# Kernel optimization log

Measured on AMD Instinct MI355X. Metric: run time of the kernel, lower is better.

Reference implementation:

```python
import jax, jax.numpy as jnp
import numpy as np

_SQRT1_2 = 0.7071067811865476

B, S, D, N, NCH = 4, 2048, 1024, 32768, 8


def setup_inputs() -> dict:
    key = jax.random.key(0)
    ks = jax.random.split(key, 6)
    return {
        "x": jax.random.normal(ks[0], (B, S, D), jnp.float32),
        "h": jax.random.normal(ks[1], (B, S, D), jnp.float32),
        "emb": jax.random.normal(ks[2], (N, D), jnp.float32),
        "tau_offset": jax.random.normal(ks[3], (B, S, 1), jnp.float32),
        "w_read": jax.random.normal(ks[4], (N, D), jnp.float32),
        "w_write": jax.random.normal(ks[5], (N, D), jnp.float32),
        "n_chunks": NCH,
    }


def _srw_chunked(x, h, emb_unit, tau_offset, w_read, w_write, n_chunks):
    b, s, d = x.shape
    n = emb_unit.shape[0]
    cs = n // n_chunks
    h_bf = h.astype(jnp.bfloat16)
    x_bf = x.astype(jnp.bfloat16)
    emb_bf = emb_unit.astype(jnp.bfloat16)
    read_bf = w_read.astype(jnp.bfloat16)
    write_bf = w_write.astype(jnp.bfloat16)
    z1 = jnp.zeros((b, s, 1), jnp.float32)

    # ---- pass 1: online score statistics over chunks of N ----
    @jax.checkpoint
    def stats_step(carry, i):
        s_sum, sq_sum, cube_sum, ns_sum, ns_sq = carry
        ec = jax.lax.dynamic_slice_in_dim(emb_bf, i * cs, cs, axis=0)
        sc = (h_bf @ ec.T).astype(jnp.float32)  # [B,S,cs]
        s_sum = s_sum + sc.sum(-1, keepdims=True)
        sq_sum = sq_sum + (sc ** 2).sum(-1, keepdims=True)
        cube_sum = cube_sum + (sc ** 3).sum(-1, keepdims=True)
        pns = sc.mean(axis=(0, 1))  # per-neuron mean score [cs]
        return ((s_sum, sq_sum, cube_sum, ns_sum + pns.sum(), ns_sq + (pns ** 2).sum()), None)

    (s_sum, sq_sum, cube_sum, ns_sum, ns_sq), _ = jax.lax.scan(
        stats_step, (z1, z1, z1, jnp.float32(0.0), jnp.float32(0.0)), jnp.arange(n_chunks))

    s_mean = s_sum / n
    s_std = jnp.sqrt(sq_sum / n - s_mean ** 2) + 1e-08
    tau = s_mean + tau_offset * s_std
    cube_mean = cube_sum / n
    central_third = cube_mean - 3.0 * s_mean * s_std ** 2 - s_mean ** 3
    score_skew = jax.lax.stop_gradient((central_third / (s_std ** 3 + 1e-08)).mean())
    mean_score = ns_sum / n
    var_score = ns_sq / n - mean_score ** 2
    score_lb = var_score / (mean_score ** 2 + var_score + 0.01)

    # ---- pass 2: erf-threshold gate + read/write GEMM accumulate ----
    @jax.checkpoint
    def gate_step(carry, i):
        out, wcost, gmax, act, strong, phib, zsum, z075c, z030c, glg = carry
        s0 = i * cs
        ec = jax.lax.dynamic_slice_in_dim(emb_bf, s0, cs, axis=0)
        rc = jax.lax.dynamic_slice_in_dim(read_bf, s0, cs, axis=0)
        wc = jax.lax.dynamic_slice_in_dim(write_bf, s0, cs, axis=0)
        rc = rc / (jnp.linalg.norm(rc, axis=-1, keepdims=True) + 1e-08)
        wc = wc / (jnp.linalg.norm(wc, axis=-1, keepdims=True) + 1e-08)
        z = ((h_bf @ ec.T).astype(jnp.float32) - tau) / s_std  # [B,S,cs]
        phi = 0.5 * (1.0 + jax.lax.erf(z * _SQRT1_2))
        gate = jnp.where(z > 0, z * phi, 0.0)
        xr = x_bf @ rc.T  # [B,S,cs]
        c_out = ((gate.astype(jnp.bfloat16) * xr) @ wc).astype(jnp.float32)  # [B,S,D]
        g_safe = gate + 1e-08
        new = (
            out + c_out,
            wcost + gate.sum(-1, keepdims=True),
            jnp.maximum(gmax, gate.max(-1, keepdims=True)),
            act + (gate > 0.0).astype(jnp.float32).sum(-1, keepdims=True),
            strong + (gate > 0.5).astype(jnp.float32).sum(-1, keepdims=True),
            phib + ((phi > 0.95) | (phi < 0.05)).astype(jnp.float32).sum(-1, keepdims=True),
            zsum + jnp.where(z > 0, z, 0.0).sum(-1, keepdims=True),
            z075c + ((z > 0) & (z < 0.75)).astype(jnp.float32).sum(-1, keepdims=True),
            z030c + ((z > 0) & (z < 0.3)).astype(jnp.float32).sum(-1, keepdims=True),
            glg + (gate * jnp.log(g_safe)).sum(-1, keepdims=True),
        )
        return (new, None)

    init = (jnp.zeros((b, s, d), jnp.float32), z1, jnp.full((b, s, 1), -1e9, jnp.float32),
            z1, z1, z1, z1, z1, z1, z1)
    (raw_out, wcost, gmax, act, strong, phib, zsum, z075c, z030c, glg), _ = jax.lax.scan(
        gate_step, init, jnp.arange(n_chunks))

    den = jnp.maximum(wcost, 1.0)
    out = (raw_out / den).astype(jnp.bfloat16)
    score_std_out = s_std.mean()
    es_out = wcost.mean()
    active_n_mean = act.mean()
    z_mean_active = zsum / (act + 1e-08)
    active_eps = act + 1e-08
    z_lt_075_frac = jax.lax.stop_gradient((z075c / active_eps).mean())
    z_lt_030_frac = jax.lax.stop_gradient((z030c / active_eps).mean())
    tau_abs_mean = jax.lax.stop_gradient(tau).mean()
    active_per_token_std = jax.lax.stop_gradient(act).std()
    gate_sum_eps = wcost + 1e-08
    entropy_per_token = -glg / gate_sum_eps + jnp.log(gate_sum_eps)
    gate_entropy = jax.lax.stop_gradient(entropy_per_token).mean()
    return (out.astype(jnp.float32), act / n, gmax, score_lb, score_std_out, es_out,
            active_n_mean, strong / n, phib / n, z_mean_active, tau_abs_mean,
            z_lt_075_frac, z_lt_030_frac, score_skew, active_per_token_std, gate_entropy)


def reference(x, h, emb, tau_offset, w_read, w_write, n_chunks):
    emb_unit = emb / (jnp.linalg.norm(emb, axis=-1, keepdims=True) + 1e-08)
    return _srw_chunked(x, h, emb_unit, tau_offset, w_read, w_write, n_chunks)
```

## Files before the change

kernel.cpp:

```cpp
#include <hip/hip_runtime.h>

#define DEV __device__ __forceinline__

typedef __attribute__((ext_vector_type(4))) float f32x4;
typedef __attribute__((ext_vector_type(8))) short s16x8;
typedef __attribute__((ext_vector_type(8))) unsigned short u16x8;

static const int NTOK = 8192;
static const int DD   = 1024;
static const int NNEU = 32768;
static const int NC   = 8192;

static const int OUT_ACT    = 8388608;
static const int OUT_GMAX   = 8396800;
static const int OUT_SLB    = 8404992;
static const int OUT_SSTD   = 8404993;
static const int OUT_ES     = 8404994;
static const int OUT_ANM    = 8404995;
static const int OUT_STRONG = 8404996;
static const int OUT_PHIB   = 8413188;
static const int OUT_ZMEAN  = 8421380;
static const int OUT_TAUM   = 8429572;
static const int OUT_Z75    = 8429573;
static const int OUT_Z30    = 8429574;
static const int OUT_SKEW   = 8429575;
static const int OUT_ASTD   = 8429576;
static const int OUT_ENT    = 8429577;

DEV unsigned short f2bf(float f){
  unsigned u = __float_as_uint(f);
  u += 0x7fffu + ((u >> 16) & 1u);
  return (unsigned short)(u >> 16);
}
DEV float bf2f(unsigned short h){ return __uint_as_float(((unsigned)h) << 16); }
DEV float rnd_bf(float f){ return bf2f(f2bf(f)); }

template<int AUX>
DEV void gl_lds16(const void* g, void* l){
  __builtin_amdgcn_global_load_lds(
      (const __attribute__((address_space(1))) unsigned int*)g,
      (__attribute__((address_space(3))) unsigned int*)l, 16, 0, AUX);
}

DEV f32x4 mfma16(s16x8 a, s16x8 b, f32x4 c){
  return __builtin_amdgcn_mfma_f32_16x16x32_bf16(a, b, c, 0, 0, 0);
}

template<int AUX>
DEV void stage4(const unsigned short* __restrict__ G, size_t ld, int k0,
                unsigned short* L, int t){
  #pragma unroll
  for (int i = 0; i < 4; i++){
    int ch = i*256 + t;
    int row = ch >> 3, c = ch & 7;
    int cs = c ^ (row & 7);
    int wb = (i*256 + (t & 192)) * 16;
    gl_lds16<AUX>(G + (size_t)row * ld + k0 + cs*8, (char*)L + wb);
  }
}

DEV s16x8 frg(const unsigned short* L, int R, int kk, int lq){
  int cc = ((kk >> 3) + lq) ^ (R & 7);
  return *(const s16x8*)((const char*)L + R*128 + cc*16);
}

DEV void waitv_bar(){
  asm volatile("s_waitcnt vmcnt(0)" ::: "memory");
  __builtin_amdgcn_s_barrier();
  __builtin_amdgcn_sched_barrier(0);
}

DEV int2 xcd_remap(){
  int orig = blockIdx.y * gridDim.x + blockIdx.x;
  int nwg  = gridDim.x * gridDim.y;
  int q = nwg >> 3;
  int xcd = orig & 7, idx = orig >> 3;
  int pos = xcd * q + idx;
  int2 r; r.x = pos >> 6; r.y = pos & 63;
  return r;
}


__global__ __launch_bounds__(256) void k_norms(const float* __restrict__ e,
    const float* __restrict__ r_, const float* __restrict__ w_,
    float* __restrict__ inv_e, float* __restrict__ inv_r, float* __restrict__ inv_w){
  int t = threadIdx.x, l = t & 63, wv = t >> 6;
  int row = blockIdx.x * 4 + wv;
  const float4* ep = (const float4*)(e  + (size_t)row * DD);
  const float4* rp = (const float4*)(r_ + (size_t)row * DD);
  const float4* wp = (const float4*)(w_ + (size_t)row * DD);
  float se = 0.f, sr = 0.f, sw = 0.f;
  #pragma unroll
  for (int j = 0; j < 4; j++){
    float4 v = ep[j*64 + l];
    se += v.x*v.x + v.y*v.y + v.z*v.z + v.w*v.w;
    float4 a = rp[j*64 + l];
    float a0 = rnd_bf(a.x), a1 = rnd_bf(a.y), a2 = rnd_bf(a.z), a3 = rnd_bf(a.w);
    sr += a0*a0 + a1*a1 + a2*a2 + a3*a3;
    float4 c = wp[j*64 + l];
    float c0 = rnd_bf(c.x), c1 = rnd_bf(c.y), c2 = rnd_bf(c.z), c3 = rnd_bf(c.w);
    sw += c0*c0 + c1*c1 + c2*c2 + c3*c3;
  }
  #pragma unroll
  for (int d = 1; d < 64; d <<= 1){
    se += __shfl_xor(se, d); sr += __shfl_xor(sr, d); sw += __shfl_xor(sw, d);
  }
  if (l == 0){
    inv_e[row] = 1.f / (sqrtf(se) + 1e-8f);
    inv_r[row] = 1.f / (sqrtf(sr) + 1e-8f);
    inv_w[row] = 1.f / (sqrtf(sw) + 1e-8f);
  }
}

__global__ __launch_bounds__(256) void k_cast_scale(const float* __restrict__ in,
    const float* __restrict__ inv, unsigned short* __restrict__ o, int round_first){
  size_t i = (size_t)blockIdx.x * 256 + threadIdx.x;
  int row = (int)(i >> 8);
  float s = inv[row];
  float4 v = ((const float4*)in)[i];
  ushort4 r;
  if (round_first){
    r.x = f2bf(rnd_bf(v.x) * s); r.y = f2bf(rnd_bf(v.y) * s);
    r.z = f2bf(rnd_bf(v.z) * s); r.w = f2bf(rnd_bf(v.w) * s);
  } else {
    r.x = f2bf(v.x * s); r.y = f2bf(v.y * s);
    r.z = f2bf(v.z * s); r.w = f2bf(v.w * s);
  }
  ((ushort4*)o)[i] = r;
}

__global__ __launch_bounds__(256) void k_cast(const float* __restrict__ in,
                                              unsigned short* __restrict__ o){
  size_t i = (size_t)blockIdx.x * 256 + threadIdx.x;
  float4 v = ((const float4*)in)[i];
  ushort4 r;
  r.x = f2bf(v.x); r.y = f2bf(v.y); r.z = f2bf(v.z); r.w = f2bf(v.w);
  ((ushort4*)o)[i] = r;
}

__global__ __launch_bounds__(256) void k_wcnT(const float* __restrict__ w_,
    const float* __restrict__ invw, unsigned short* __restrict__ o){
  __shared__ unsigned short tile[64][65];
  int t = threadIdx.x;
  int n0b = blockIdx.x * 64, d0 = blockIdx.y * 64;
  #pragma unroll
  for (int i = 0; i < 16; i++){
    int idx = t + i*256;
    int r = idx >> 6, c = idx & 63;
    float v = w_[(size_t)(n0b + r) * DD + d0 + c];
    tile[c][r] = f2bf(rnd_bf(v) * invw[n0b + r]);
  }
  __syncthreads();
  #pragma unroll
  for (int i = 0; i < 16; i++){
    int idx = t + i*256;
    int rd = idx >> 6, cn = idx & 63;
    o[(size_t)(d0 + rd) * NNEU + n0b + cn] = tile[rd][cn];
  }
}

__global__ __launch_bounds__(256) void k_hsum(const unsigned short* __restrict__ hb,
                                              float* __restrict__ hs){
  int t = threadIdx.x; int r0 = blockIdx.x * 128;
  float s[4] = {0.f, 0.f, 0.f, 0.f};
  for (int r = 0; r < 128; r++){
    const unsigned short* row = hb + (size_t)(r0 + r) * DD;
    #pragma unroll
    for (int j = 0; j < 4; j++) s[j] += bf2f(row[j*256 + t]);
  }
  #pragma unroll
  for (int j = 0; j < 4; j++) atomicAdd(hs + j*256 + t, s[j]);
}

__global__ __launch_bounds__(256) void k_pns(const unsigned short* __restrict__ eb,
    const float* __restrict__ hs, float* __restrict__ ns){
  __shared__ float hsh[1024];
  __shared__ float pr[8];
  int t = threadIdx.x, l = t & 63, wv = t >> 6;
  for (int i = t; i < 1024; i += 256) hsh[i] = hs[i];
  __syncthreads();
  float bs = 0.f, bq = 0.f;
  for (int it = 0; it < 32; it++){
    int row = blockIdx.x * 128 + it*4 + wv;
    const unsigned short* er = eb + (size_t)row * DD + l*16;
    float s = 0.f;
    #pragma unroll
    for (int j = 0; j < 16; j++) s += hsh[l*16 + j] * bf2f(er[j]);
    #pragma unroll
    for (int d = 1; d < 64; d <<= 1) s += __shfl_xor(s, d);
    float pns = s * (1.f / 8192.f);
    bs += pns; bq += pns * pns;
  }
  if (l == 0){ pr[wv*2] = bs; pr[wv*2 + 1] = bq; }
  __syncthreads();
  if (t == 0){
    atomicAdd(ns + 0, pr[0] + pr[2] + pr[4] + pr[6]);
    atomicAdd(ns + 1, pr[1] + pr[3] + pr[5] + pr[7]);
  }
}


__global__ __launch_bounds__(256, 2) void k_stats_gemm(
    const unsigned short* __restrict__ A, const unsigned short* __restrict__ Bm,
    float* __restrict__ s_sum, float* __restrict__ sq_sum, float* __restrict__ cu_sum,
    unsigned short* __restrict__ Sb, int kst)
{
  __shared__ unsigned short lds[32768];
  const int t = threadIdx.x, l = t & 63, wv = t >> 6;
  const int wm = wv >> 1, wn = wv & 1;
  const int lq = l >> 4, lr = l & 15;
  int2 rm = xcd_remap();
  const int bx = rm.x, by = rm.y;
  const unsigned short* Ab = A  + (size_t)by * 128 * DD;
  const unsigned short* Bb = Bm + (size_t)bx * 128 * DD;
  f32x4 acc[4][4];
  #pragma unroll
  for (int m = 0; m < 4; m++)
    #pragma unroll
    for (int n = 0; n < 4; n++) acc[m][n] = (f32x4){0.f, 0.f, 0.f, 0.f};

  stage4<0>(Ab, DD, 0, lds, t);
  stage4<0>(Bb, DD, 0, lds + 8192, t);
  waitv_bar();
  int cur = 0;
  for (int ks = 0; ks < 16; ++ks){
    unsigned short* Lc = lds + cur*16384;
    if (ks + 1 < 16){
      unsigned short* Ln = lds + (cur^1)*16384;
      int k0 = (ks+1)*64;
      stage4<0>(Ab, DD, k0, Ln, t);
      stage4<0>(Bb, DD, k0, Ln + 8192, t);
    }
    #pragma unroll
    for (int kk = 0; kk < 64; kk += 32){
      s16x8 af[4], bf4[4];
      #pragma unroll
      for (int m = 0; m < 4; m++) af[m]  = frg(Lc, wm*64 + m*16 + lr, kk, lq);
      #pragma unroll
      for (int n = 0; n < 4; n++) bf4[n] = frg(Lc + 8192, wn*64 + n*16 + lr, kk, lq);
      #pragma unroll
      for (int m = 0; m < 4; m++)
        #pragma unroll
        for (int n = 0; n < 4; n++)
          acc[m][n] = mfma16(af[m], bf4[n], acc[m][n]);
    }
    waitv_bar();
    cur ^= 1;
  }

  int ci = bx >> 6;
  if (ci < kst){
    unsigned short* sl = lds;
    #pragma unroll
    for (int m = 0; m < 4; m++)
    #pragma unroll
    for (int n = 0; n < 4; n++)
    #pragma unroll
    for (int r = 0; r < 4; r++){
      int rl = wm*64 + m*16 + lq*4 + r;
      int cl = wn*64 + n*16 + lr;
      sl[rl*136 + cl] = f2bf(acc[m][n][r]);
    }
    __syncthreads();
    unsigned short* Sp = Sb + (size_t)ci * NTOK * NC;
    int bxc = bx & 63;
    #pragma unroll
    for (int i = 0; i < 8; i++){
      int idx = i*2048 + t*8;
      int row = idx >> 7, col = idx & 127;
      u16x8 v = *(const u16x8*)&sl[row*136 + col];
      __builtin_nontemporal_store(v,
        (u16x8*)(Sp + (size_t)(by*128 + row) * NC + bxc*128 + col));
    }
  }
  __syncthreads();

  float* red = (float*)lds;
  #pragma unroll
  for (int m = 0; m < 4; m++)
  #pragma unroll
  for (int r = 0; r < 4; r++){
    float s1 = 0.f, s2 = 0.f, s3 = 0.f;
    #pragma unroll
    for (int n = 0; n < 4; n++){
      float v = rnd_bf(acc[m][n][r]);
      s1 += v; float v2 = v*v; s2 += v2; s3 += v2*v;
    }
    #pragma unroll
    for (int d = 1; d < 16; d <<= 1){
      s1 += __shfl_xor(s1, d); s2 += __shfl_xor(s2, d); s3 += __shfl_xor(s3, d);
    }
    if (lr == 0){
      int rl = wm*64 + m*16 + lq*4 + r;
      float* p = red + (wn*128 + rl)*4;
      p[0] = s1; p[1] = s2; p[2] = s3;
    }
  }
  __syncthreads();
  const int row0 = by * 128;
  for (int idx = t; idx < 384; idx += 256){
    int rl = idx / 3, st = idx - rl*3;
    float v = red[rl*4 + st] + red[(128 + rl)*4 + st];
    float* dst = (st == 0) ? s_sum : (st == 1) ? sq_sum : cu_sum;
    atomicAdd(dst + row0 + rl, v);
  }
}

__global__ __launch_bounds__(256) void k_tau(const float* __restrict__ s_sum,
    const float* __restrict__ sq_sum, const float* __restrict__ tof,
    float* __restrict__ tau, float* __restrict__ rstd){
  int i = blockIdx.x * 256 + threadIdx.x;
  float mean = s_sum[i] * (1.f / 32768.f);
  float var  = sq_sum[i] * (1.f / 32768.f) - mean*mean;
  float sstd = sqrtf(fmaxf(var, 0.f)) + 1e-8f;
  tau[i]  = mean + tof[i] * sstd;
  rstd[i] = 1.f / sstd;
}


__global__ __launch_bounds__(256, 2) void k_gateS(
    const unsigned short* __restrict__ Xb, const unsigned short* __restrict__ Rb,
    const float* __restrict__ tau, const float* __restrict__ rstd,
    unsigned short* __restrict__ SP, int n0,
    float* __restrict__ wcostp, float* __restrict__ gmaxp, float* __restrict__ actp,
    float* __restrict__ strongp, float* __restrict__ phibp, float* __restrict__ zsump,
    float* __restrict__ z075p, float* __restrict__ z030p, float* __restrict__ glgp)
{
  __shared__ unsigned short lds[32768];
  const int t = threadIdx.x, l = t & 63, wv = t >> 6;
  const int wm = wv >> 1, wn = wv & 1;
  const int lq = l >> 4, lr = l & 15;
  int2 rm = xcd_remap();
  const int bx = rm.x, by = rm.y;
  const unsigned short* Xp = Xb + (size_t)by * 128 * DD;
  const unsigned short* Rp = Rb + (size_t)(n0 + bx*128) * DD;
  f32x4 accX[4][4];
  #pragma unroll
  for (int m = 0; m < 4; m++)
    #pragma unroll
    for (int n = 0; n < 4; n++) accX[m][n] = (f32x4){0.f,0.f,0.f,0.f};

  stage4<0>(Xp, DD, 0, lds, t);
  stage4<0>(Rp, DD, 0, lds + 8192, t);
  waitv_bar();
  int cur = 0;
  for (int ks = 0; ks < 16; ++ks){
    unsigned short* Lc = lds + cur*16384;
    if (ks + 1 < 16){
      unsigned short* Ln = lds + (cur^1)*16384;
      int k0 = (ks+1)*64;
      stage4<0>(Xp, DD, k0, Ln, t);
      stage4<0>(Rp, DD, k0, Ln + 8192, t);
    }
    #pragma unroll
    for (int kk = 0; kk < 64; kk += 32){
      s16x8 af[4], bf4[4];
      #pragma unroll
      for (int m = 0; m < 4; m++) af[m]  = frg(Lc, wm*64 + m*16 + lr, kk, lq);
      #pragma unroll
      for (int n = 0; n < 4; n++) bf4[n] = frg(Lc + 8192, wn*64 + n*16 + lr, kk, lq);
      #pragma unroll
      for (int m = 0; m < 4; m++)
        #pragma unroll
        for (int n = 0; n < 4; n++)
          accX[m][n] = mfma16(af[m], bf4[n], accX[m][n]);
    }
    waitv_bar();
    cur ^= 1;
  }

  unsigned short sv[4][4][4];
  #pragma unroll
  for (int m = 0; m < 4; m++)
  #pragma unroll
  for (int r = 0; r < 4; r++)
  #pragma unroll
  for (int n = 0; n < 4; n++){
    int gr = by*128 + wm*64 + m*16 + lq*4 + r;
    int gc = bx*128 + wn*64 + n*16 + lr;
    sv[m][r][n] = SP[(size_t)gr * NC + gc];
  }

  __syncthreads();
  float* red = (float*)lds;
  #pragma unroll
  for (int m = 0; m < 4; m++)
  #pragma unroll
  for (int r = 0; r < 4; r++){
    int rl = wm*64 + m*16 + lq*4 + r;
    int gr = by*128 + rl;
    float tauv = tau[gr], rs = rstd[gr];
    float wsum = 0.f, gmx = 0.f, ac = 0.f, stc = 0.f, pb = 0.f;
    float zs = 0.f, z7 = 0.f, z3 = 0.f, gl = 0.f;
    #pragma unroll
    for (int n = 0; n < 4; n++){
      float sc = bf2f(sv[m][r][n]);
      float xr = rnd_bf(accX[m][n][r]);
      float z = (sc - tauv) * rs;
      float phi = 0.5f * (1.0f + erff(z * 0.70710678118654752440f));
      float gate = (z > 0.f) ? z * phi : 0.f;
      wsum += gate; gmx = fmaxf(gmx, gate);
      if (gate > 0.f)  ac  += 1.f;
      if (gate > 0.5f) stc += 1.f;
      if (phi > 0.95f || phi < 0.05f) pb += 1.f;
      if (z > 0.f){ zs += z; if (z < 0.75f) z7 += 1.f; if (z < 0.3f) z3 += 1.f; }
      gl += gate * __logf(gate + 1e-8f);
      float p = rnd_bf(gate) * xr;
      SP[(size_t)gr * NC + bx*128 + wn*64 + n*16 + lr] = f2bf(p);
    }
    #pragma unroll
    for (int d = 1; d < 16; d <<= 1){
      wsum += __shfl_xor(wsum, d); gmx = fmaxf(gmx, __shfl_xor(gmx, d));
      ac += __shfl_xor(ac, d);  stc += __shfl_xor(stc, d); pb += __shfl_xor(pb, d);
      zs += __shfl_xor(zs, d);  z7  += __shfl_xor(z7, d);  z3 += __shfl_xor(z3, d);
      gl += __shfl_xor(gl, d);
    }
    if (lr == 0){
      float* p = red + (wn*128 + rl)*10;
      p[0]=wsum; p[1]=gmx; p[2]=ac; p[3]=stc; p[4]=pb; p[5]=zs; p[6]=z7; p[7]=z3; p[8]=gl;
    }
  }
  __syncthreads();
  for (int idx = t; idx < 1152; idx += 256){
    int rl = idx / 9, st = idx - rl*9;
    float a = red[rl*10 + st], b = red[(128 + rl)*10 + st];
    int gr = by*128 + rl;
    if (st == 1){
      atomicMax((int*)(gmaxp + gr), __float_as_int(fmaxf(a, b)));
    } else {
      float v = a + b;
      float* dst = (st==0)?wcostp:(st==2)?actp:(st==3)?strongp:(st==4)?phibp:
                   (st==5)?zsump:(st==6)?z075p:(st==7)?z030p:glgp;
      atomicAdd(dst + gr, v);
    }
  }
}


__global__ __launch_bounds__(256, 2) void k_gate_gemm(
    const unsigned short* __restrict__ Hb, const unsigned short* __restrict__ Eb,
    const unsigned short* __restrict__ Xb, const unsigned short* __restrict__ Rb,
    const float* __restrict__ tau, const float* __restrict__ rstd,
    unsigned short* __restrict__ P, int n0,
    float* __restrict__ wcostp, float* __restrict__ gmaxp, float* __restrict__ actp,
    float* __restrict__ strongp, float* __restrict__ phibp, float* __restrict__ zsump,
    float* __restrict__ z075p, float* __restrict__ z030p, float* __restrict__ glgp)
{
  __shared__ unsigned short lds[32768];
  unsigned short* lH = lds;
  unsigned short* lE = lds + 8192;
  unsigned short* lX = lds + 16384;
  unsigned short* lR = lds + 24576;
  const int t = threadIdx.x, l = t & 63, wv = t >> 6;
  const int wm = wv >> 1, wn = wv & 1;
  const int lq = l >> 4, lr = l & 15;
  int2 rm = xcd_remap();
  const int bx = rm.x, by = rm.y;
  const unsigned short* Hp = Hb + (size_t)by * 128 * DD;
  const unsigned short* Xp = Xb + (size_t)by * 128 * DD;
  const unsigned short* Ep = Eb + (size_t)(n0 + bx*128) * DD;
  const unsigned short* Rp = Rb + (size_t)(n0 + bx*128) * DD;
  f32x4 accS[4][4], accX[4][4];
  #pragma unroll
  for (int m = 0; m < 4; m++)
    #pragma unroll
    for (int n = 0; n < 4; n++){
      accS[m][n] = (f32x4){0.f,0.f,0.f,0.f};
      accX[m][n] = (f32x4){0.f,0.f,0.f,0.f};
    }

  for (int k0 = 0; k0 < DD; k0 += 64){
    __syncthreads();
    stage4<0>(Hp, DD, k0, lH, t);
    stage4<0>(Ep, DD, k0, lE, t);
    stage4<0>(Xp, DD, k0, lX, t);
    stage4<0>(Rp, DD, k0, lR, t);
    asm volatile("s_waitcnt vmcnt(0)" ::: "memory");
    __syncthreads();
    #pragma unroll
    for (int kk = 0; kk < 64; kk += 32){
      s16x8 af[4], bf4[4];
      #pragma unroll
      for (int m = 0; m < 4; m++) af[m]  = frg(lH, wm*64 + m*16 + lr, kk, lq);
      #pragma unroll
      for (int n = 0; n < 4; n++) bf4[n] = frg(lE, wn*64 + n*16 + lr, kk, lq);
      #pragma unroll
      for (int m = 0; m < 4; m++)
        #pragma unroll
        for (int n = 0; n < 4; n++)
          accS[m][n] = mfma16(af[m], bf4[n], accS[m][n]);
      #pragma unroll
      for (int m = 0; m < 4; m++) af[m]  = frg(lX, wm*64 + m*16 + lr, kk, lq);
      #pragma unroll
      for (int n = 0; n < 4; n++) bf4[n] = frg(lR, wn*64 + n*16 + lr, kk, lq);
      #pragma unroll
      for (int m = 0; m < 4; m++)
        #pragma unroll
        for (int n = 0; n < 4; n++)
          accX[m][n] = mfma16(af[m], bf4[n], accX[m][n]);
    }
  }
  __syncthreads();
  float* red = (float*)lds;
  #pragma unroll
  for (int m = 0; m < 4; m++)
  #pragma unroll
  for (int r = 0; r < 4; r++){
    int rl = wm*64 + m*16 + lq*4 + r;
    int gr = by*128 + rl;
    float tauv = tau[gr], rs = rstd[gr];
    float wsum = 0.f, gmx = 0.f, ac = 0.f, stc = 0.f, pb = 0.f;
    float zs = 0.f, z7 = 0.f, z3 = 0.f, gl = 0.f;
    #pragma unroll
    for (int n = 0; n < 4; n++){
      float sc = rnd_bf(accS[m][n][r]);
      float xr = rnd_bf(accX[m][n][r]);
      float z = (sc - tauv) * rs;
      float phi = 0.5f * (1.0f + erff(z * 0.70710678118654752440f));
      float gate = (z > 0.f) ? z * phi : 0.f;
      wsum += gate; gmx = fmaxf(gmx, gate);
      if (gate > 0.f)  ac  += 1.f;
      if (gate > 0.5f) stc += 1.f;
      if (phi > 0.95f || phi < 0.05f) pb += 1.f;
      if (z > 0.f){ zs += z; if (z < 0.75f) z7 += 1.f; if (z < 0.3f) z3 += 1.f; }
      gl += gate * __logf(gate + 1e-8f);
      float p = rnd_bf(gate) * xr;
      P[(size_t)gr * NC + bx*128 + wn*64 + n*16 + lr] = f2bf(p);
    }
    #pragma unroll
    for (int d = 1; d < 16; d <<= 1){
      wsum += __shfl_xor(wsum, d); gmx = fmaxf(gmx, __shfl_xor(gmx, d));
      ac += __shfl_xor(ac, d);  stc += __shfl_xor(stc, d); pb += __shfl_xor(pb, d);
      zs += __shfl_xor(zs, d);  z7  += __shfl_xor(z7, d);  z3 += __shfl_xor(z3, d);
      gl += __shfl_xor(gl, d);
    }
    if (lr == 0){
      float* p = red + (wn*128 + rl)*10;
      p[0]=wsum; p[1]=gmx; p[2]=ac; p[3]=stc; p[4]=pb; p[5]=zs; p[6]=z7; p[7]=z3; p[8]=gl;
    }
  }
  __syncthreads();
  for (int idx = t; idx < 1152; idx += 256){
    int rl = idx / 9, st = idx - rl*9;
    float a = red[rl*10 + st], b = red[(128 + rl)*10 + st];
    int gr = by*128 + rl;
    if (st == 1){
      atomicMax((int*)(gmaxp + gr), __float_as_int(fmaxf(a, b)));
    } else {
      float v = a + b;
      float* dst = (st==0)?wcostp:(st==2)?actp:(st==3)?strongp:(st==4)?phibp:
                   (st==5)?zsump:(st==6)?z075p:(st==7)?z030p:glgp;
      atomicAdd(dst + gr, v);
    }
  }
}


__global__ __launch_bounds__(256, 2) void k_out_gemm(
    const unsigned short* __restrict__ Pm, const unsigned short* __restrict__ Bt,
    float* __restrict__ outp, int n0, int accum)
{
  __shared__ unsigned short lds[32768];
  const int t = threadIdx.x, l = t & 63, wv = t >> 6;
  const int wm = wv >> 1, wn = wv & 1;
  const int lq = l >> 4, lr = l & 15;
  int2 rm = xcd_remap();
  const int bx = rm.x, by = rm.y;
  const unsigned short* Ab = Pm + (size_t)by * 128 * NC;
  const unsigned short* Bb = Bt + (size_t)bx * 128 * NNEU + n0;
  f32x4 acc[4][4];
  #pragma unroll
  for (int m = 0; m < 4; m++)
    #pragma unroll
    for (int n = 0; n < 4; n++) acc[m][n] = (f32x4){0.f,0.f,0.f,0.f};

  const int NT = NC / 64;
  stage4<2>(Ab, NC, 0, lds, t);
  stage4<0>(Bb, NNEU, 0, lds + 8192, t);
  waitv_bar();
  int cur = 0;
  for (int ks = 0; ks < NT; ++ks){
    unsigned short* Lc = lds + cur*16384;
    if (ks + 1 < NT){
      unsigned short* Ln = lds + (cur^1)*16384;
      int k0 = (ks+1)*64;
      stage4<2>(Ab, NC, k0, Ln, t);
      stage4<0>(Bb, NNEU, k0, Ln + 8192, t);
    }
    #pragma unroll
    for (int kk = 0; kk < 64; kk += 32){
      s16x8 af[4], bf4[4];
      #pragma unroll
      for (int m = 0; m < 4; m++) af[m]  = frg(Lc, wm*64 + m*16 + lr, kk, lq);
      #pragma unroll
      for (int n = 0; n < 4; n++) bf4[n] = frg(Lc + 8192, wn*64 + n*16 + lr, kk, lq);
      #pragma unroll
      for (int m = 0; m < 4; m++)
        #pragma unroll
        for (int n = 0; n < 4; n++)
          acc[m][n] = mfma16(af[m], bf4[n], acc[m][n]);
    }
    waitv_bar();
    cur ^= 1;
  }
  #pragma unroll
  for (int m = 0; m < 4; m++)
  #pragma unroll
  for (int n = 0; n < 4; n++)
  #pragma unroll
  for (int r = 0; r < 4; r++){
    int gr = by*128 + wm*64 + m*16 + lq*4 + r;
    int dc = bx*128 + wn*64 + n*16 + lr;
    float* o = outp + (size_t)gr * DD + dc;
    if (accum) *o += acc[m][n][r];
    else       *o  = acc[m][n][r];
  }
}


__global__ __launch_bounds__(256) void k_out_fin(float* __restrict__ o,
                                                 const float* __restrict__ wcost){
  size_t i = (size_t)blockIdx.x * 256 + threadIdx.x;
  float4 v = ((const float4*)o)[i];
  int tk = (int)(i >> 8);
  float den = fmaxf(wcost[tk], 1.f);
  v.x = rnd_bf(v.x / den); v.y = rnd_bf(v.y / den);
  v.z = rnd_bf(v.z / den); v.w = rnd_bf(v.w / den);
  ((float4*)o)[i] = v;
}

__global__ __launch_bounds__(1024) void k_final(
    const float* __restrict__ s_sum, const float* __restrict__ sq_sum,
    const float* __restrict__ cu_sum, const float* __restrict__ tof,
    const float* __restrict__ wcost, const float* __restrict__ gmax,
    const float* __restrict__ act, const float* __restrict__ strong,
    const float* __restrict__ phib, const float* __restrict__ zsum,
    const float* __restrict__ z075, const float* __restrict__ z030,
    const float* __restrict__ glg, const float* __restrict__ ns,
    float* __restrict__ out)
{
  int tid = threadIdx.x;
  float s0=0,s1=0,s2=0,s3=0,s4=0,s5=0,s6=0,s7=0,s8=0;
  for (int i = tid; i < NTOK; i += 1024){
    float mean = s_sum[i] * (1.f / 32768.f);
    float var  = sq_sum[i] * (1.f / 32768.f) - mean*mean;
    float sstd = sqrtf(fmaxf(var, 0.f)) + 1e-8f;
    float tauv = mean + tof[i] * sstd;
    float wc = wcost[i], ac = act[i];
    out[OUT_ACT + i]    = ac * (1.f / 32768.f);
    out[OUT_GMAX + i]   = gmax[i];
    out[OUT_STRONG + i] = strong[i] * (1.f / 32768.f);
    out[OUT_PHIB + i]   = phib[i] * (1.f / 32768.f);
    out[OUT_ZMEAN + i]  = zsum[i] / (ac + 1e-8f);
    float c3 = cu_sum[i] * (1.f / 32768.f) - 3.f*mean*sstd*sstd - mean*mean*mean;
    float skew = c3 / (sstd*sstd*sstd + 1e-8f);
    float gse = wc + 1e-8f;
    float ent = -glg[i] / gse + logf(gse);
    s0 += sstd; s1 += wc; s2 += ac; s3 += ac*ac; s4 += tauv;
    s5 += z075[i] / (ac + 1e-8f); s6 += z030[i] / (ac + 1e-8f); s7 += skew; s8 += ent;
  }
  __shared__ float rb[16][9];
  int lane = tid & 63, wid = tid >> 6;
  #pragma unroll
  for (int d = 1; d < 64; d <<= 1){
    s0 += __shfl_xor(s0,d); s1 += __shfl_xor(s1,d); s2 += __shfl_xor(s2,d);
    s3 += __shfl_xor(s3,d); s4 += __shfl_xor(s4,d); s5 += __shfl_xor(s5,d);
    s6 += __shfl_xor(s6,d); s7 += __shfl_xor(s7,d); s8 += __shfl_xor(s8,d);
  }
  if (lane == 0){
    rb[wid][0]=s0; rb[wid][1]=s1; rb[wid][2]=s2; rb[wid][3]=s3; rb[wid][4]=s4;
    rb[wid][5]=s5; rb[wid][6]=s6; rb[wid][7]=s7; rb[wid][8]=s8;
  }
  __syncthreads();
  if (tid == 0){
    float S[9];
    for (int k = 0; k < 9; k++){ float a = 0.f; for (int w2 = 0; w2 < 16; w2++) a += rb[w2][k]; S[k] = a; }
    const float inv = 1.f / 8192.f;
    float act_mean = S[2] * inv;
    out[OUT_SSTD] = S[0] * inv;
    out[OUT_ES]   = S[1] * inv;
    out[OUT_ANM]  = act_mean;
    out[OUT_ASTD] = sqrtf(fmaxf(S[3]*inv - act_mean*act_mean, 0.f));
    out[OUT_TAUM] = S[4] * inv;
    out[OUT_Z75]  = S[5] * inv;
    out[OUT_Z30]  = S[6] * inv;
    out[OUT_SKEW] = S[7] * inv;
    out[OUT_ENT]  = S[8] * inv;
    float ms = ns[0] * (1.f / 32768.f);
    float vs = ns[1] * (1.f / 32768.f) - ms*ms;
    out[OUT_SLB] = vs / (ms*ms + vs + 0.01f);
  }
}


extern "C" void kernel_launch(void* const* d_in, const int* in_sizes, int n_in,
                              void* d_out, int out_size, void* d_ws, size_t ws_size,
                              hipStream_t stream)
{
  (void)in_sizes; (void)n_in; (void)out_size;
  const float* x   = (const float*)d_in[0];
  const float* h   = (const float*)d_in[1];
  const float* emb = (const float*)d_in[2];
  const float* tof = (const float*)d_in[3];
  const float* wr  = (const float*)d_in[4];
  const float* ww  = (const float*)d_in[5];
  float* out = (float*)d_out;
  char* ws = (char*)d_ws;

  size_t off = 0;
  auto get = [&](size_t n){ size_t o = off; off += (n + 255) & ~(size_t)255; return o; };
  unsigned short* rcn_bf = (unsigned short*)(ws + get((size_t)NNEU*DD*2));
  unsigned short* h_bf   = (unsigned short*)(ws + get((size_t)NTOK*DD*2));
  unsigned short* x_bf   = (unsigned short*)(ws + get((size_t)NTOK*DD*2));
  float* inv_e = (float*)(ws + get(NNEU*4));
  float* inv_r = (float*)(ws + get(NNEU*4));
  float* inv_w = (float*)(ws + get(NNEU*4));
  size_t zoff = off;
  float* hsum   = (float*)(ws + get(DD*4));
  float* s_sum  = (float*)(ws + get(NTOK*4));
  float* sq_sum = (float*)(ws + get(NTOK*4));
  float* cu_sum = (float*)(ws + get(NTOK*4));
  float* tau    = (float*)(ws + get(NTOK*4));
  float* rstd   = (float*)(ws + get(NTOK*4));
  float* wcost  = (float*)(ws + get(NTOK*4));
  float* gmax   = (float*)(ws + get(NTOK*4));
  float* act    = (float*)(ws + get(NTOK*4));
  float* strong = (float*)(ws + get(NTOK*4));
  float* phib   = (float*)(ws + get(NTOK*4));
  float* zsum   = (float*)(ws + get(NTOK*4));
  float* z075   = (float*)(ws + get(NTOK*4));
  float* z030   = (float*)(ws + get(NTOK*4));
  float* glg    = (float*)(ws + get(NTOK*4));
  float* ns     = (float*)(ws + get(256));
  size_t zlen = off - zoff;
  unsigned short* emb_bf = (unsigned short*)(ws + get((size_t)NNEU*DD*2));

  const size_t szS = (size_t)NTOK * NC * 2;
  unsigned short* wcnT;
  int kst;
  size_t poff;
  size_t poffA = (off + 4095) & ~(size_t)4095;
  size_t availA = ws_size > poffA ? ws_size - poffA : 0;
  if (availA >= 4*szS){
    wcnT = emb_bf;
    kst = 4; poff = poffA;
  } else {
    wcnT = (unsigned short*)(ws + get((size_t)DD*NNEU*2));
    poff = (off + 4095) & ~(size_t)4095;
    size_t avail = ws_size > poff ? ws_size - poff : 0;
    kst = (int)(avail / szS); if (kst > 4) kst = 4;
  }
  unsigned short* Sb = (unsigned short*)(ws + poff);

  hipMemsetAsync(ws + zoff, 0, zlen, stream);

  dim3 b256(256);
  k_norms<<<dim3(NNEU/4), b256, 0, stream>>>(emb, wr, ww, inv_e, inv_r, inv_w);
  k_cast_scale<<<dim3(NNEU*DD/4/256), b256, 0, stream>>>(emb, inv_e, emb_bf, 0);
  k_cast_scale<<<dim3(NNEU*DD/4/256), b256, 0, stream>>>(wr, inv_r, rcn_bf, 1);
  k_cast<<<dim3(NTOK*DD/4/256), b256, 0, stream>>>(h, h_bf);
  k_cast<<<dim3(NTOK*DD/4/256), b256, 0, stream>>>(x, x_bf);
  k_hsum<<<dim3(NTOK/128), b256, 0, stream>>>(h_bf, hsum);
  k_pns<<<dim3(NNEU/128), b256, 0, stream>>>(emb_bf, hsum, ns);
  k_stats_gemm<<<dim3(NNEU/128, NTOK/128), b256, 0, stream>>>(h_bf, emb_bf,
      s_sum, sq_sum, cu_sum, Sb, kst);
  k_tau<<<dim3(NTOK/256), b256, 0, stream>>>(s_sum, sq_sum, tof, tau, rstd);
  k_wcnT<<<dim3(NNEU/64, DD/64), b256, 0, stream>>>(ww, inv_w, wcnT);

  for (int c = 0; c < 4; ++c){
    int reg = (kst > 0) ? (c < kst ? c : (c % kst)) : 0;
    unsigned short* Pc = Sb + (size_t)reg * NTOK * NC;
    if (c < kst){
      k_gateS<<<dim3(NC/128, NTOK/128), b256, 0, stream>>>(x_bf, rcn_bf,
          tau, rstd, Pc, c*NC, wcost, gmax, act, strong, phib, zsum, z075, z030, glg);
    } else {
      k_gate_gemm<<<dim3(NC/128, NTOK/128), b256, 0, stream>>>(h_bf, emb_bf, x_bf, rcn_bf,
          tau, rstd, Pc, c*NC, wcost, gmax, act, strong, phib, zsum, z075, z030, glg);
    }
    k_out_gemm<<<dim3(DD/128, NTOK/128), b256, 0, stream>>>(Pc, wcnT, out, c*NC, c);
  }
  k_out_fin<<<dim3(NTOK*DD/4/256), b256, 0, stream>>>(out, wcost);
  k_final<<<dim3(1), dim3(1024), 0, stream>>>(s_sum, sq_sum, cu_sum, tof, wcost, gmax,
      act, strong, phib, zsum, z075, z030, glg, ns, out);
}
```

Before: 4.023 ms.

## Split score GEMM per chunk, tile-swizzle blocks, stage gate stores through LDS

Replaces the whole-N stats GEMM with per-chunk score launches and uses an 8x8 tile-grouped XCD remap for better L2 reuse. Drops the fused dual-GEMM fallback in favor of recomputing scores into a slot. Gate outputs are now staged in LDS and written with coalesced vector stores, and output normalization is fused into the last out GEMM, removing a separate pass. The wcnT buffer is always allocated separately, which may reduce how many score slots fit in the workspace.

```diff
diff --git a/kernel.cpp b/kernel.cpp
--- a/kernel.cpp
+++ b/kernel.cpp
@@ -70,13 +70,13 @@
   __builtin_amdgcn_sched_barrier(0);
 }
 
-DEV int2 xcd_remap(){
-  int orig = blockIdx.y * gridDim.x + blockIdx.x;
-  int nwg  = gridDim.x * gridDim.y;
-  int q = nwg >> 3;
-  int xcd = orig & 7, idx = orig >> 3;
-  int pos = xcd * q + idx;
-  int2 r; r.x = pos >> 6; r.y = pos & 63;
+DEV int2 xcd64(){
+  int orig = blockIdx.y * 64 + blockIdx.x;
+  int xcd = orig & 7, p = orig >> 3;
+  int sqy = p >> 6, off = p & 63;
+  int2 r;
+  r.x = xcd*8 + (off & 7);
+  r.y = sqy*8 + (off >> 3);
   return r;
 }
 
@@ -200,16 +200,17 @@
 }
 
 
-__global__ __launch_bounds__(256, 2) void k_stats_gemm(
+template<bool DO_STATS>
+__global__ __launch_bounds__(256, 2) void k_score(
     const unsigned short* __restrict__ A, const unsigned short* __restrict__ Bm,
     float* __restrict__ s_sum, float* __restrict__ sq_sum, float* __restrict__ cu_sum,
-    unsigned short* __restrict__ Sb, int kst)
+    unsigned short* __restrict__ Sout, int do_store)
 {
   __shared__ unsigned short lds[32768];
   const int t = threadIdx.x, l = t & 63, wv = t >> 6;
   const int wm = wv >> 1, wn = wv & 1;
   const int lq = l >> 4, lr = l & 15;
-  int2 rm = xcd_remap();
+  int2 rm = xcd64();
   const int bx = rm.x, by = rm.y;
   const unsigned short* Ab = A  + (size_t)by * 128 * DD;
   const unsigned short* Bb = Bm + (size_t)bx * 128 * DD;
@@ -248,9 +249,10 @@
     cur ^= 1;
   }
 
-  int ci = bx >> 6;
-  if (ci < kst){
-    unsigned short* sl = lds;
+  unsigned short* sl = lds;
+  float* red = (float*)((char*)lds + 49152);
+
+  if (do_store){
     #pragma unroll
     for (int m = 0; m < 4; m++)
     #pragma unroll
@@ -261,48 +263,47 @@
       int cl = wn*64 + n*16 + lr;
       sl[rl*136 + cl] = f2bf(acc[m][n][r]);
     }
-    __syncthreads();
-    unsigned short* Sp = Sb + (size_t)ci * NTOK * NC;
-    int bxc = bx & 63;
+  }
+  if (DO_STATS){
+    #pragma unroll
+    for (int m = 0; m < 4; m++)
+    #pragma unroll
+    for (int r = 0; r < 4; r++){
+      float s1 = 0.f, s2 = 0.f, s3 = 0.f;
+      #pragma unroll
+      for (int n = 0; n < 4; n++){
+        float v = rnd_bf(acc[m][n][r]);
+        s1 += v; float v2 = v*v; s2 += v2; s3 += v2*v;
+      }
+      #pragma unroll
+      for (int d = 1; d < 16; d <<= 1){
+        s1 += __shfl_xor(s1, d); s2 += __shfl_xor(s2, d); s3 += __shfl_xor(s3, d);
+      }
+      if (lr == 0){
+        int rl = wm*64 + m*16 + lq*4 + r;
+        float* p = red + (wn*128 + rl)*4;
+        p[0] = s1; p[1] = s2; p[2] = s3;
+      }
+    }
+  }
+  __syncthreads();
+  if (do_store){
     #pragma unroll
     for (int i = 0; i < 8; i++){
       int idx = i*2048 + t*8;
       int row = idx >> 7, col = idx & 127;
       u16x8 v = *(const u16x8*)&sl[row*136 + col];
-      __builtin_nontemporal_store(v,
-        (u16x8*)(Sp + (size_t)(by*128 + row) * NC + bxc*128 + col));
-    }
-  }
-  __syncthreads();
-
-  float* red = (float*)lds;
-  #pragma unroll
-  for (int m = 0; m < 4; m++)
-  #pragma unroll
-  for (int r = 0; r < 4; r++){
-    float s1 = 0.f, s2 = 0.f, s3 = 0.f;
-    #pragma unroll
-    for (int n = 0; n < 4; n++){
-      float v = rnd_bf(acc[m][n][r]);
-      s1 += v; float v2 = v*v; s2 += v2; s3 += v2*v;
-    }
-    #pragma unroll
-    for (int d = 1; d < 16; d <<= 1){
-      s1 += __shfl_xor(s1, d); s2 += __shfl_xor(s2, d); s3 += __shfl_xor(s3, d);
-    }
-    if (lr == 0){
-      int rl = wm*64 + m*16 + lq*4 + r;
-      float* p = red + (wn*128 + rl)*4;
-      p[0] = s1; p[1] = s2; p[2] = s3;
-    }
-  }
-  __syncthreads();
-  const int row0 = by * 128;
-  for (int idx = t; idx < 384; idx += 256){
-    int rl = idx / 3, st = idx - rl*3;
-    float v = red[rl*4 + st] + red[(128 + rl)*4 + st];
-    float* dst = (st == 0) ? s_sum : (st == 1) ? sq_sum : cu_sum;
-    atomicAdd(dst + row0 + rl, v);
+      *(u16x8*)(Sout + (size_t)(by*128 + row) * NC + bx*128 + col) = v;
+    }
+  }
+  if (DO_STATS){
+    const int row0 = by * 128;
+    for (int idx = t; idx < 384; idx += 256){
+      int rl = idx / 3, st = idx - rl*3;
+      float v = red[rl*4 + st] + red[(128 + rl)*4 + st];
+      float* dst = (st == 0) ? s_sum : (st == 1) ? sq_sum : cu_sum;
+      atomicAdd(dst + row0 + rl, v);
+    }
   }
 }
 
@@ -330,7 +331,7 @@
   const int t = threadIdx.x, l = t & 63, wv = t >> 6;
   const int wm = wv >> 1, wn = wv & 1;
   const int lq = l >> 4, lr = l & 15;
-  int2 rm = xcd_remap();
+  int2 rm = xcd64();
   const int bx = rm.x, by = rm.y;
   const unsigned short* Xp = Xb + (size_t)by * 128 * DD;
   const unsigned short* Rp = Rb + (size_t)(n0 + bx*128) * DD;
@@ -381,8 +382,9 @@
     sv[m][r][n] = SP[(size_t)gr * NC + gc];
   }
 
-  __syncthreads();
-  float* red = (float*)lds;
+  unsigned short* plds = lds;
+  float* red = (float*)((char*)lds + 49152);
+
   #pragma unroll
   for (int m = 0; m < 4; m++)
   #pragma unroll
@@ -406,7 +408,7 @@
       if (z > 0.f){ zs += z; if (z < 0.75f) z7 += 1.f; if (z < 0.3f) z3 += 1.f; }
       gl += gate * __logf(gate + 1e-8f);
       float p = rnd_bf(gate) * xr;
-      SP[(size_t)gr * NC + bx*128 + wn*64 + n*16 + lr] = f2bf(p);
+      plds[rl*136 + wn*64 + n*16 + lr] = f2bf(p);
     }
     #pragma unroll
     for (int d = 1; d < 16; d <<= 1){
@@ -421,6 +423,13 @@
     }
   }
   __syncthreads();
+  #pragma unroll
+  for (int i = 0; i < 8; i++){
+    int idx = i*2048 + t*8;
+    int row = idx >> 7, col = idx & 127;
+    u16x8 v = *(const u16x8*)&plds[row*136 + col];
+    *(u16x8*)(SP + (size_t)(by*128 + row) * NC + bx*128 + col) = v;
+  }
   for (int idx = t; idx < 1152; idx += 256){
     int rl = idx / 9, st = idx - rl*9;
     float a = red[rl*10 + st], b = red[(128 + rl)*10 + st];
@@ -437,137 +446,17 @@
 }
 
 
-__global__ __launch_bounds__(256, 2) void k_gate_gemm(
-    const unsigned short* __restrict__ Hb, const unsigned short* __restrict__ Eb,
-    const unsigned short* __restrict__ Xb, const unsigned short* __restrict__ Rb,
-    const float* __restrict__ tau, const float* __restrict__ rstd,
-    unsigned short* __restrict__ P, int n0,
-    float* __restrict__ wcostp, float* __restrict__ gmaxp, float* __restrict__ actp,
-    float* __restrict__ strongp, float* __restrict__ phibp, float* __restrict__ zsump,
-    float* __restrict__ z075p, float* __restrict__ z030p, float* __restrict__ glgp)
-{
-  __shared__ unsigned short lds[32768];
-  unsigned short* lH = lds;
-  unsigned short* lE = lds + 8192;
-  unsigned short* lX = lds + 16384;
-  unsigned short* lR = lds + 24576;
-  const int t = threadIdx.x, l = t & 63, wv = t >> 6;
-  const int wm = wv >> 1, wn = wv & 1;
-  const int lq = l >> 4, lr = l & 15;
-  int2 rm = xcd_remap();
-  const int bx = rm.x, by = rm.y;
-  const unsigned short* Hp = Hb + (size_t)by * 128 * DD;
-  const unsigned short* Xp = Xb + (size_t)by * 128 * DD;
-  const unsigned short* Ep = Eb + (size_t)(n0 + bx*128) * DD;
-  const unsigned short* Rp = Rb + (size_t)(n0 + bx*128) * DD;
-  f32x4 accS[4][4], accX[4][4];
-  #pragma unroll
-  for (int m = 0; m < 4; m++)
-    #pragma unroll
-    for (int n = 0; n < 4; n++){
-      accS[m][n] = (f32x4){0.f,0.f,0.f,0.f};
-      accX[m][n] = (f32x4){0.f,0.f,0.f,0.f};
-    }
-
-  for (int k0 = 0; k0 < DD; k0 += 64){
-    __syncthreads();
-    stage4<0>(Hp, DD, k0, lH, t);
-    stage4<0>(Ep, DD, k0, lE, t);
-    stage4<0>(Xp, DD, k0, lX, t);
-    stage4<0>(Rp, DD, k0, lR, t);
-    asm volatile("s_waitcnt vmcnt(0)" ::: "memory");
-    __syncthreads();
-    #pragma unroll
-    for (int kk = 0; kk < 64; kk += 32){
-      s16x8 af[4], bf4[4];
-      #pragma unroll
-      for (int m = 0; m < 4; m++) af[m]  = frg(lH, wm*64 + m*16 + lr, kk, lq);
-      #pragma unroll
-      for (int n = 0; n < 4; n++) bf4[n] = frg(lE, wn*64 + n*16 + lr, kk, lq);
-      #pragma unroll
-      for (int m = 0; m < 4; m++)
-        #pragma unroll
-        for (int n = 0; n < 4; n++)
-          accS[m][n] = mfma16(af[m], bf4[n], accS[m][n]);
-      #pragma unroll
-      for (int m = 0; m < 4; m++) af[m]  = frg(lX, wm*64 + m*16 + lr, kk, lq);
-      #pragma unroll
-      for (int n = 0; n < 4; n++) bf4[n] = frg(lR, wn*64 + n*16 + lr, kk, lq);
-      #pragma unroll
-      for (int m = 0; m < 4; m++)
-        #pragma unroll
-        for (int n = 0; n < 4; n++)
-          accX[m][n] = mfma16(af[m], bf4[n], accX[m][n]);
-    }
-  }
-  __syncthreads();
-  float* red = (float*)lds;
-  #pragma unroll
-  for (int m = 0; m < 4; m++)
-  #pragma unroll
-  for (int r = 0; r < 4; r++){
-    int rl = wm*64 + m*16 + lq*4 + r;
-    int gr = by*128 + rl;
-    float tauv = tau[gr], rs = rstd[gr];
-    float wsum = 0.f, gmx = 0.f, ac = 0.f, stc = 0.f, pb = 0.f;
-    float zs = 0.f, z7 = 0.f, z3 = 0.f, gl = 0.f;
-    #pragma unroll
-    for (int n = 0; n < 4; n++){
-      float sc = rnd_bf(accS[m][n][r]);
-      float xr = rnd_bf(accX[m][n][r]);
-      float z = (sc - tauv) * rs;
-      float phi = 0.5f * (1.0f + erff(z * 0.70710678118654752440f));
-      float gate = (z > 0.f) ? z * phi : 0.f;
-      wsum += gate; gmx = fmaxf(gmx, gate);
-      if (gate > 0.f)  ac  += 1.f;
-      if (gate > 0.5f) stc += 1.f;
-      if (phi > 0.95f || phi < 0.05f) pb += 1.f;
-      if (z > 0.f){ zs += z; if (z < 0.75f) z7 += 1.f; if (z < 0.3f) z3 += 1.f; }
-      gl += gate * __logf(gate + 1e-8f);
-      float p = rnd_bf(gate) * xr;
-      P[(size_t)gr * NC + bx*128 + wn*64 + n*16 + lr] = f2bf(p);
-    }
-    #pragma unroll
-    for (int d = 1; d < 16; d <<= 1){
-      wsum += __shfl_xor(wsum, d); gmx = fmaxf(gmx, __shfl_xor(gmx, d));
-      ac += __shfl_xor(ac, d);  stc += __shfl_xor(stc, d); pb += __shfl_xor(pb, d);
-      zs += __shfl_xor(zs, d);  z7  += __shfl_xor(z7, d);  z3 += __shfl_xor(z3, d);
-      gl += __shfl_xor(gl, d);
-    }
-    if (lr == 0){
-      float* p = red + (wn*128 + rl)*10;
-      p[0]=wsum; p[1]=gmx; p[2]=ac; p[3]=stc; p[4]=pb; p[5]=zs; p[6]=z7; p[7]=z3; p[8]=gl;
-    }
-  }
-  __syncthreads();
-  for (int idx = t; idx < 1152; idx += 256){
-    int rl = idx / 9, st = idx - rl*9;
-    float a = red[rl*10 + st], b = red[(128 + rl)*10 + st];
-    int gr = by*128 + rl;
-    if (st == 1){
-      atomicMax((int*)(gmaxp + gr), __float_as_int(fmaxf(a, b)));
-    } else {
-      float v = a + b;
-      float* dst = (st==0)?wcostp:(st==2)?actp:(st==3)?strongp:(st==4)?phibp:
-                   (st==5)?zsump:(st==6)?z075p:(st==7)?z030p:glgp;
-      atomicAdd(dst + gr, v);
-    }
-  }
-}
-
-
 __global__ __launch_bounds__(256, 2) void k_out_gemm(
     const unsigned short* __restrict__ Pm, const unsigned short* __restrict__ Bt,
-    float* __restrict__ outp, int n0, int accum)
+    float* __restrict__ outp, const float* __restrict__ wcost, int accum, int fin)
 {
   __shared__ unsigned short lds[32768];
   const int t = threadIdx.x, l = t & 63, wv = t >> 6;
   const int wm = wv >> 1, wn = wv & 1;
   const int lq = l >> 4, lr = l & 15;
-  int2 rm = xcd_remap();
-  const int bx = rm.x, by = rm.y;
+  const int bx = blockIdx.x, by = blockIdx.y;
   const unsigned short* Ab = Pm + (size_t)by * 128 * NC;
-  const unsigned short* Bb = Bt + (size_t)bx * 128 * NNEU + n0;
+  const unsigned short* Bb = Bt + (size_t)bx * 128 * NNEU;
   f32x4 acc[4][4];
   #pragma unroll
   for (int m = 0; m < 4; m++)
@@ -606,28 +495,21 @@
   #pragma unroll
   for (int m = 0; m < 4; m++)
   #pragma unroll
-  for (int n = 0; n < 4; n++)
-  #pragma unroll
   for (int r = 0; r < 4; r++){
     int gr = by*128 + wm*64 + m*16 + lq*4 + r;
-    int dc = bx*128 + wn*64 + n*16 + lr;
-    float* o = outp + (size_t)gr * DD + dc;
-    if (accum) *o += acc[m][n][r];
-    else       *o  = acc[m][n][r];
-  }
-}
-
-
-__global__ __launch_bounds__(256) void k_out_fin(float* __restrict__ o,
-                                                 const float* __restrict__ wcost){
-  size_t i = (size_t)blockIdx.x * 256 + threadIdx.x;
-  float4 v = ((const float4*)o)[i];
-  int tk = (int)(i >> 8);
-  float den = fmaxf(wcost[tk], 1.f);
-  v.x = rnd_bf(v.x / den); v.y = rnd_bf(v.y / den);
-  v.z = rnd_bf(v.z / den); v.w = rnd_bf(v.w / den);
-  ((float4*)o)[i] = v;
-}
+    float den = fin ? fmaxf(wcost[gr], 1.f) : 1.f;
+    #pragma unroll
+    for (int n = 0; n < 4; n++){
+      int dc = bx*128 + wn*64 + n*16 + lr;
+      float* o = outp + (size_t)gr * DD + dc;
+      float v = acc[m][n][r];
+      if (accum) v += *o;
+      if (fin)   v = rnd_bf(v / den);
+      *o = v;
+    }
+  }
+}
+
 
 __global__ __launch_bounds__(1024) void k_final(
     const float* __restrict__ s_sum, const float* __restrict__ sq_sum,
@@ -710,6 +592,8 @@
   size_t off = 0;
   auto get = [&](size_t n){ size_t o = off; off += (n + 255) & ~(size_t)255; return o; };
   unsigned short* rcn_bf = (unsigned short*)(ws + get((size_t)NNEU*DD*2));
+  unsigned short* emb_bf = (unsigned short*)(ws + get((size_t)NNEU*DD*2));
+  unsigned short* wcnT   = (unsigned short*)(ws + get((size_t)DD*NNEU*2));
   unsigned short* h_bf   = (unsigned short*)(ws + get((size_t)NTOK*DD*2));
   unsigned short* x_bf   = (unsigned short*)(ws + get((size_t)NTOK*DD*2));
   float* inv_e = (float*)(ws + get(NNEU*4));
@@ -733,28 +617,19 @@
   float* glg    = (float*)(ws + get(NTOK*4));
   float* ns     = (float*)(ws + get(256));
   size_t zlen = off - zoff;
-  unsigned short* emb_bf = (unsigned short*)(ws + get((size_t)NNEU*DD*2));
 
   const size_t szS = (size_t)NTOK * NC * 2;
-  unsigned short* wcnT;
-  int kst;
-  size_t poff;
-  size_t poffA = (off + 4095) & ~(size_t)4095;
-  size_t availA = ws_size > poffA ? ws_size - poffA : 0;
-  if (availA >= 4*szS){
-    wcnT = emb_bf;
-    kst = 4; poff = poffA;
-  } else {
-    wcnT = (unsigned short*)(ws + get((size_t)DD*NNEU*2));
-    poff = (off + 4095) & ~(size_t)4095;
-    size_t avail = ws_size > poff ? ws_size - poff : 0;
-    kst = (int)(avail / szS); if (kst > 4) kst = 4;
-  }
+  size_t poff = (off + 4095) & ~(size_t)4095;
+  size_t avail = ws_size > poff ? ws_size - poff : 0;
+  int kst = (int)(avail / szS);
+  if (kst > 4) kst = 4;
+  if (kst < 1) kst = 1;
   unsigned short* Sb = (unsigned short*)(ws + poff);
 
   hipMemsetAsync(ws + zoff, 0, zlen, stream);
 
   dim3 b256(256);
+  dim3 gC(64, 64);
   k_norms<<<dim3(NNEU/4), b256, 0, stream>>>(emb, wr, ww, inv_e, inv_r, inv_w);
   k_cast_scale<<<dim3(NNEU*DD/4/256), b256, 0, stream>>>(emb, inv_e, emb_bf, 0);
   k_cast_scale<<<dim3(NNEU*DD/4/256), b256, 0, stream>>>(wr, inv_r, rcn_bf, 1);
@@ -762,24 +637,27 @@
   k_cast<<<dim3(NTOK*DD/4/256), b256, 0, stream>>>(x, x_bf);
   k_hsum<<<dim3(NTOK/128), b256, 0, stream>>>(h_bf, hsum);
   k_pns<<<dim3(NNEU/128), b256, 0, stream>>>(emb_bf, hsum, ns);
-  k_stats_gemm<<<dim3(NNEU/128, NTOK/128), b256, 0, stream>>>(h_bf, emb_bf,
-      s_sum, sq_sum, cu_sum, Sb, kst);
+
+  for (int c = 0; c < 4; ++c){
+    unsigned short* slot = Sb + (size_t)(c < kst ? c : 0) * NTOK * NC;
+    k_score<true><<<gC, b256, 0, stream>>>(h_bf, emb_bf + (size_t)c*NC*DD,
+        s_sum, sq_sum, cu_sum, slot, c < kst ? 1 : 0);
+  }
   k_tau<<<dim3(NTOK/256), b256, 0, stream>>>(s_sum, sq_sum, tof, tau, rstd);
   k_wcnT<<<dim3(NNEU/64, DD/64), b256, 0, stream>>>(ww, inv_w, wcnT);
 
   for (int c = 0; c < 4; ++c){
-    int reg = (kst > 0) ? (c < kst ? c : (c % kst)) : 0;
-    unsigned short* Pc = Sb + (size_t)reg * NTOK * NC;
-    if (c < kst){
-      k_gateS<<<dim3(NC/128, NTOK/128), b256, 0, stream>>>(x_bf, rcn_bf,
-          tau, rstd, Pc, c*NC, wcost, gmax, act, strong, phib, zsum, z075, z030, glg);
-    } else {
-      k_gate_gemm<<<dim3(NC/128, NTOK/128), b256, 0, stream>>>(h_bf, emb_bf, x_bf, rcn_bf,
-          tau, rstd, Pc, c*NC, wcost, gmax, act, strong, phib, zsum, z075, z030, glg);
-    }
-    k_out_gemm<<<dim3(DD/128, NTOK/128), b256, 0, stream>>>(Pc, wcnT, out, c*NC, c);
-  }
-  k_out_fin<<<dim3(NTOK*DD/4/256), b256, 0, stream>>>(out, wcost);
+    int slot_i = (c < kst) ? c : (c % kst);
+    unsigned short* slot = Sb + (size_t)slot_i * NTOK * NC;
+    if (c >= kst){
+      k_score<false><<<gC, b256, 0, stream>>>(h_bf, emb_bf + (size_t)c*NC*DD,
+          nullptr, nullptr, nullptr, slot, 1);
+    }
+    k_gateS<<<gC, b256, 0, stream>>>(x_bf, rcn_bf, tau, rstd, slot, c*NC,
+        wcost, gmax, act, strong, phib, zsum, z075, z030, glg);
+    k_out_gemm<<<dim3(DD/128, NTOK/128), b256, 0, stream>>>(slot, wcnT + (size_t)c*NC,
+        out, wcost, c > 0 ? 1 : 0, c == 3 ? 1 : 0);
+  }
   k_final<<<dim3(1), dim3(1024), 0, stream>>>(s_sum, sq_sum, cu_sum, tof, wcost, gmax,
       act, strong, phib, zsum, z075, z030, glg, ns, out);
 }
```

After: 4.649 ms. 1.16x slower.
